# Kernel optimization log

Hardware: AMD Instinct MI355X
Metric: run time of the kernel (lower is better)

The kernel has to match this reference:

```python
import jax, jax.numpy as jnp
import numpy as np

H = 64  # hidden width hard-coded in Agent body


def setup_inputs() -> dict:
    key = jax.random.key(0)
    ks = jax.random.split(key, 10)
    T, B, OBS, A = 1024, 512, 128, 18
    x = jax.random.normal(ks[0], (T, B, OBS), dtype=jnp.float32)
    mask = jax.random.bernoulli(ks[1], 0.01, (T, B))
    initial_carry = jnp.zeros((B, H), dtype=jnp.float32)
    s = lambda k, sh: (jax.random.normal(k, sh, dtype=jnp.float32) * 0.05)
    W1 = s(ks[2], (OBS, H)); b1 = jnp.zeros((H,), jnp.float32)
    Wi = s(ks[3], (H, 3 * H)); bi = jnp.zeros((3 * H,), jnp.float32)
    Wh = s(ks[4], (H, 3 * H)); bhn = jnp.zeros((H,), jnp.float32)
    W2 = s(ks[5], (H, H)); b2 = jnp.zeros((H,), jnp.float32)
    Wl = s(ks[6], (H, A)); bl = jnp.zeros((A,), jnp.float32)
    Wv = s(ks[7], (H, 1)); bv = jnp.zeros((1,), jnp.float32)
    return dict(x=x, mask=mask, initial_carry=initial_carry,
                W1=W1, b1=b1, Wi=Wi, bi=bi, Wh=Wh, bhn=bhn,
                W2=W2, b2=b2, Wl=Wl, bl=bl, Wv=Wv, bv=bv)


def _gru(h, z_t, Wi, bi, Wh, bhn):
    # flax nn.GRUCell math
    gi = z_t @ Wi + bi            # [B, 3H]
    gh = h @ Wh                   # [B, 3H]
    ir, iz, inn = jnp.split(gi, 3, axis=-1)
    hr, hz, hn = jnp.split(gh, 3, axis=-1)
    r = jax.nn.sigmoid(ir + hr)
    u = jax.nn.sigmoid(iz + hz)
    n = jnp.tanh(inn + r * (hn + bhn))
    return (1.0 - u) * n + u * h


def reference(x, mask, initial_carry, W1, b1, Wi, bi, Wh, bhn, W2, b2, Wl, bl, Wv, bv):
    # stem: Dense(64) + relu, applied to all timesteps at once
    z = jax.nn.relu(x @ W1 + b1)                  # [T, B, H]
    m = mask[..., None]                           # [T, B, 1]

    def step(h, inp):
        z_t, m_t = inp
        # masked reset of the carry at episode boundaries
        h = jnp.where(m_t, initial_carry, h)
        h = _gru(h, z_t, Wi, bi, Wh, bhn)
        return h, h

    h_final, ys = jax.lax.scan(step, initial_carry, (z, m))  # ys: [T, B, H]

    y = jax.nn.relu(ys @ W2 + b2)                 # [T, B, H]
    logits = y @ Wl + bl                          # [T, B, A]
    value = y @ Wv + bv                           # [T, B, 1]
    return h_final, logits.squeeze(), value.squeeze(-1)
```

## Files before the change

kernel.cpp:

```cpp
#include <hip/hip_runtime.h>
#include <stdint.h>

#define TT  1024
#define BB  512
#define OBS 128
#define HH  64
#define AA  18
#define RT  (TT*BB)
#define OFF_L ((size_t)BB*HH)
#define OFF_V (OFF_L + (size_t)TT*BB*AA)

#define GI_ELEMS ((size_t)RT*192)
#define WS_NEED  ((GI_ELEMS + (size_t)RT*HH)*4)

typedef __attribute__((ext_vector_type(8))) short bf16x8;
typedef __attribute__((ext_vector_type(4))) float f32x4;
typedef __attribute__((ext_vector_type(4))) unsigned int u32x4;

__device__ __forceinline__ float fast_rcp(float x){ return __builtin_amdgcn_rcpf(x); }
__device__ __forceinline__ float sigm(float x){ return fast_rcp(1.f + __expf(-x)); }
__device__ __forceinline__ float tanh_(float x){ return 1.f - 2.f*fast_rcp(1.f + __expf(2.f*x)); }

__device__ __forceinline__ unsigned bf16_rne(float f){
    unsigned u = __float_as_uint(f);
    return (u + 0x7FFFu + ((u>>16)&1u)) >> 16;
}
__device__ __forceinline__ unsigned pk_bf16(float lo, float hi){
    unsigned d;
    asm("v_cvt_pk_bf16_f32 %0, %1, %2" : "=v"(d) : "v"(lo), "v"(hi));
    return d;
}

__global__ void detect_mask(const uint32_t* __restrict__ m, uint32_t* __restrict__ flag)
{
    const int n_words = (TT * BB) / 4;
    uint32_t acc = 0;
    for (int i = blockIdx.x * blockDim.x + threadIdx.x; i < n_words;
         i += gridDim.x * blockDim.x)
        acc |= (m[i] > 1u) ? 1u : 0u;
    if (acc) flag[0] = 1u;
}

#define P1_BLOCKS 1024
#define ZSTR 70

__global__ __launch_bounds__(256, 2)
void stem_gi(const float* __restrict__ x,
             const float* __restrict__ W1, const float* __restrict__ b1,
             const float* __restrict__ Wi, const float* __restrict__ bi,
             float* __restrict__ gi)
{
    const int tid = threadIdx.x, w = tid >> 6, l = tid & 63;
    const int a = l & 15, q = l >> 4;

    __shared__ float z_s[4][16*ZSTR];
    float* zw = &z_s[w][0];

    bf16x8 W1f[4][4];
    #pragma unroll
    for (int nt = 0; nt < 4; ++nt)
        #pragma unroll
        for (int kf = 0; kf < 4; ++kf) {
            u32x4 pk;
            #pragma unroll
            for (int j2 = 0; j2 < 4; ++j2) {
                const int k0 = kf*32 + q*8 + 2*j2;
                pk[j2] = bf16_rne(W1[(size_t)k0*HH + nt*16 + a])
                       | (bf16_rne(W1[(size_t)(k0+1)*HH + nt*16 + a]) << 16);
            }
            W1f[nt][kf] = __builtin_bit_cast(bf16x8, pk);
        }
    float b1v[4];
    #pragma unroll
    for (int nt = 0; nt < 4; ++nt) b1v[nt] = b1[nt*16 + a];

    bf16x8 Wif[12][2];
    #pragma unroll
    for (int tau = 0; tau < 12; ++tau)
        #pragma unroll
        for (int kf = 0; kf < 2; ++kf) {
            u32x4 pk;
            #pragma unroll
            for (int j2 = 0; j2 < 4; ++j2) {
                const int k0 = kf*32 + q*8 + 2*j2;
                pk[j2] = bf16_rne(Wi[(size_t)k0*192 + tau*16 + a])
                       | (bf16_rne(Wi[(size_t)(k0+1)*192 + tau*16 + a]) << 16);
            }
            Wif[tau][kf] = __builtin_bit_cast(bf16x8, pk);
        }
    float biv[12];
    #pragma unroll
    for (int tau = 0; tau < 12; ++tau) biv[tau] = bi[tau*16 + a];

    for (int it = 0; it < 8; ++it) {
        const size_t grp  = (size_t)blockIdx.x*32 + it*4 + w;
        const float* xr   = x + (grp*16 + a)*OBS;

        float4 xv[8];
        #pragma unroll
        for (int kf = 0; kf < 4; ++kf) {
            xv[2*kf]   = *(const float4*)(xr + kf*32 + q*8);
            xv[2*kf+1] = *(const float4*)(xr + kf*32 + q*8 + 4);
        }
        bf16x8 Af[4];
        #pragma unroll
        for (int kf = 0; kf < 4; ++kf) {
            u32x4 pk;
            pk[0] = pk_bf16(xv[2*kf].x,   xv[2*kf].y);
            pk[1] = pk_bf16(xv[2*kf].z,   xv[2*kf].w);
            pk[2] = pk_bf16(xv[2*kf+1].x, xv[2*kf+1].y);
            pk[3] = pk_bf16(xv[2*kf+1].z, xv[2*kf+1].w);
            Af[kf] = __builtin_bit_cast(bf16x8, pk);
        }

        #pragma unroll
        for (int nt = 0; nt < 4; ++nt) {
            f32x4 D = {b1v[nt], b1v[nt], b1v[nt], b1v[nt]};
            #pragma unroll
            for (int kf = 0; kf < 4; ++kf)
                D = __builtin_amdgcn_mfma_f32_16x16x32_bf16(Af[kf], W1f[nt][kf], D, 0,0,0);
            #pragma unroll
            for (int e = 0; e < 4; ++e)
                zw[(q*4 + e)*ZSTR + nt*16 + a] = fmaxf(D[e], 0.f);
        }
        bf16x8 Az[2];
        #pragma unroll
        for (int s = 0; s < 2; ++s) {
            u32x4 pk;
            #pragma unroll
            for (int j2 = 0; j2 < 4; ++j2) {
                const float2 f = *(const float2*)(zw + a*ZSTR + s*32 + q*8 + 2*j2);
                pk[j2] = pk_bf16(f.x, f.y);
            }
            Az[s] = __builtin_bit_cast(bf16x8, pk);
        }

        float* gb = gi + grp*12*256 + l*4;
        #pragma unroll
        for (int tau = 0; tau < 12; ++tau) {
            f32x4 D = {biv[tau], biv[tau], biv[tau], biv[tau]};
            D = __builtin_amdgcn_mfma_f32_16x16x32_bf16(Az[0], Wif[tau][0], D, 0,0,0);
            D = __builtin_amdgcn_mfma_f32_16x16x32_bf16(Az[1], Wif[tau][1], D, 0,0,0);
            *(f32x4*)(gb + (size_t)tau*256) = D;
        }
    }
}

__global__ __launch_bounds__(256)
void recur9(const float* __restrict__ gip,
            const void* __restrict__ mask_raw,
            const uint32_t* __restrict__ mflag,
            const float* __restrict__ ic,
            const float* __restrict__ Wh,
            const float* __restrict__ bhn,
            float* __restrict__ ys,
            float* __restrict__ out)
{
    const int blk = blockIdx.x;
    const int tid = threadIdx.x;
    const int w   = tid >> 6;
    const int l   = tid & 63;
    const int a   = l & 15;
    const int q   = l >> 4;
    const int dw  = w*16 + a;

    __shared__ float    h_lds[2][64][17];
    __shared__ uint32_t mbits[TT];

    if (mflag[0] != 0) {
        const uint8_t* m8 = (const uint8_t*)mask_raw;
        for (int t0 = w*4; t0 < TT; t0 += 16) {
            const int tt = t0 + q;
            const uint64_t bal = __ballot(m8[(size_t)tt*BB + blk*16 + a] != 0);
            if (l < 4) mbits[t0 + l] = (uint32_t)((bal >> (16*l)) & 0xFFFFu);
        }
    } else {
        const int32_t* m32 = (const int32_t*)mask_raw;
        for (int t0 = w*4; t0 < TT; t0 += 16) {
            const int tt = t0 + q;
            const uint64_t bal = __ballot(m32[(size_t)tt*BB + blk*16 + a] != 0);
            if (l < 4) mbits[t0 + l] = (uint32_t)((bal >> (16*l)) & 0xFFFFu);
        }
    }
    for (int i = tid; i < 16*64; i += 256) {
        const int c = i & 15, d = i >> 4;
        h_lds[0][d][c] = ic[(blk*16 + c)*HH + d];
    }

    bf16x8 Bf[3][2];
    #pragma unroll
    for (int g = 0; g < 3; ++g) {
        const int colb = g*64 + dw;
        #pragma unroll
        for (int s = 0; s < 2; ++s) {
            u32x4 pk;
            #pragma unroll
            for (int j2 = 0; j2 < 4; ++j2) {
                const int k0 = s*32 + q*8 + j2*2;
                pk[j2] = bf16_rne(Wh[(size_t)k0*192 + colb])
                       | (bf16_rne(Wh[(size_t)(k0+1)*192 + colb]) << 16);
            }
            Bf[g][s] = __builtin_bit_cast(bf16x8, pk);
        }
    }
    u32x4 icA[2];
    #pragma unroll
    for (int s = 0; s < 2; ++s) {
        #pragma unroll
        for (int j2 = 0; j2 < 4; ++j2) {
            const int d0 = s*32 + q*8 + j2*2;
            icA[s][j2] = bf16_rne(ic[(blk*16 + a)*HH + d0])
                       | (bf16_rne(ic[(blk*16 + a)*HH + d0 + 1]) << 16);
        }
    }
    float ic_c[4], h_reg[4];
    #pragma unroll
    for (int e = 0; e < 4; ++e) {
        ic_c[e]  = ic[(blk*16 + q*4 + e)*HH + dw];
        h_reg[e] = ic_c[e];
    }
    const float bhnv = bhn[dw];
    const f32x4 Cn = {bhnv, bhnv, bhnv, bhnv};

    __syncthreads();

    #define GSTRIDE ((size_t)32*12*256)
    const float* gbase = gip + (size_t)blk*12*256 + l*4;
    f32x4 buf0[3], buf1[3], buf2[3], buf3[3];
    #pragma unroll
    for (int g = 0; g < 3; ++g) {
        buf0[g] = *(const f32x4*)(gbase + 0*GSTRIDE + (size_t)(g*4 + w)*256);
        buf1[g] = *(const f32x4*)(gbase + 1*GSTRIDE + (size_t)(g*4 + w)*256);
        buf2[g] = *(const f32x4*)(gbase + 2*GSTRIDE + (size_t)(g*4 + w)*256);
        buf3[g] = *(const f32x4*)(gbase + 3*GSTRIDE + (size_t)(g*4 + w)*256);
    }

    auto step = [&](int t, f32x4* cur) {
        const int p = t & 1;
        const uint32_t mb = mbits[t];
        const bool mA = (mb >> a) & 1;
        u32x4 Apk0, Apk1;
        #pragma unroll
        for (int j2 = 0; j2 < 4; ++j2) {
            const int d0 = q*8 + j2*2;
            const unsigned r0 = pk_bf16(h_lds[p][d0][a],    h_lds[p][d0+1][a]);
            const unsigned r1 = pk_bf16(h_lds[p][32+d0][a], h_lds[p][32+d0+1][a]);
            Apk0[j2] = mA ? icA[0][j2] : r0;
            Apk1[j2] = mA ? icA[1][j2] : r1;
        }
        const bf16x8 A0 = __builtin_bit_cast(bf16x8, Apk0);
        const bf16x8 A1 = __builtin_bit_cast(bf16x8, Apk1);
        f32x4 Dr = __builtin_amdgcn_mfma_f32_16x16x32_bf16(A0, Bf[0][0], cur[0], 0,0,0);
        Dr       = __builtin_amdgcn_mfma_f32_16x16x32_bf16(A1, Bf[0][1], Dr,     0,0,0);
        f32x4 Dz = __builtin_amdgcn_mfma_f32_16x16x32_bf16(A0, Bf[1][0], cur[1], 0,0,0);
        Dz       = __builtin_amdgcn_mfma_f32_16x16x32_bf16(A1, Bf[1][1], Dz,     0,0,0);
        f32x4 Dn = __builtin_amdgcn_mfma_f32_16x16x32_bf16(A0, Bf[2][0], Cn,     0,0,0);
        Dn       = __builtin_amdgcn_mfma_f32_16x16x32_bf16(A1, Bf[2][1], Dn,     0,0,0);
        const f32x4 gin = cur[2];
        const int tp = (t + 4 < TT) ? (t + 4) : (TT - 1);
        #pragma unroll
        for (int g = 0; g < 3; ++g)
            cur[g] = *(const f32x4*)(gbase + (size_t)tp*GSTRIDE + (size_t)(g*4 + w)*256);
        float* ysp = ys + ((size_t)t*BB + blk*16 + q*4)*HH + dw;
        #pragma unroll
        for (int e = 0; e < 4; ++e) {
            const bool me   = (mb >> (q*4 + e)) & 1;
            const float he  = me ? ic_c[e] : h_reg[e];
            const float r   = sigm(Dr[e]);
            const float u   = sigm(Dz[e]);
            const float n   = tanh_(fmaf(r, Dn[e], gin[e]));
            const float hn  = fmaf(u, he - n, n);
            h_reg[e] = hn;
            h_lds[p ^ 1][dw][q*4 + e] = hn;
            ysp[(size_t)e*HH] = hn;
        }
        asm volatile("s_waitcnt lgkmcnt(0)" ::: "memory");
        __builtin_amdgcn_s_barrier();
    };

    for (int t = 0; t < TT; t += 4) {
        step(t,     buf0);
        step(t + 1, buf1);
        step(t + 2, buf2);
        step(t + 3, buf3);
    }
    #pragma unroll
    for (int e = 0; e < 4; ++e)
        out[(size_t)(blk*16 + q*4 + e)*HH + dw] = h_reg[e];
    #undef GSTRIDE
}

#define P3_BLOCKS 1024
#define P3_RPW (RT/(P3_BLOCKS*4))

__global__ __launch_bounds__(256, 2)
void heads(const float* __restrict__ ys,
           const float* __restrict__ W2, const float* __restrict__ b2,
           const float* __restrict__ Wl, const float* __restrict__ bl,
           const float* __restrict__ Wv, const float* __restrict__ bv,
           float* __restrict__ out)
{
    const int tid = threadIdx.x, w = tid >> 6, lane = tid & 63;
    __shared__ float4 sb[4][2][16];
    float w2r[64];
    #pragma unroll
    for (int k = 0; k < 64; ++k) w2r[k] = W2[k*HH + lane];
    const float b2v = b2[lane];
    float wc[64]; float bcv = 0.f;
    if (lane < AA) {
        #pragma unroll
        for (int k = 0; k < 64; ++k) wc[k] = Wl[k*AA + lane];
        bcv = bl[lane];
    } else if (lane == AA) {
        #pragma unroll
        for (int k = 0; k < 64; ++k) wc[k] = Wv[k];
        bcv = bv[0];
    } else {
        #pragma unroll
        for (int k = 0; k < 64; ++k) wc[k] = 0.f;
    }
    const int r0 = (blockIdx.x*4 + w) * P3_RPW;
    float ysA = ys[(size_t)r0*HH + lane];
    float ysB = ys[(size_t)(r0+1)*HH + lane];
    for (int rr = 0; rr < P3_RPW; ++rr) {
        const int row = r0 + rr;
        const float ysv = ysA;
        ysA = ysB;
        const int rn = (rr+2 < P3_RPW) ? (row+2) : (r0 + P3_RPW - 1);
        ysB = ys[(size_t)rn*HH + lane];
        ((float*)&sb[w][0][0])[lane] = ysv;
        float acc = b2v;
        {
            const float4* yb = &sb[w][0][0];
            #pragma unroll
            for (int kk = 0; kk < 16; ++kk) {
                const float4 v = yb[kk];
                acc += w2r[4*kk+0]*v.x + w2r[4*kk+1]*v.y
                     + w2r[4*kk+2]*v.z + w2r[4*kk+3]*v.w;
            }
        }
        const float yv = fmaxf(acc, 0.f);
        ((float*)&sb[w][1][0])[lane] = yv;
        float acc2 = bcv;
        {
            const float4* yb = &sb[w][1][0];
            #pragma unroll
            for (int kk = 0; kk < 16; ++kk) {
                const float4 v = yb[kk];
                acc2 += wc[4*kk+0]*v.x + wc[4*kk+1]*v.y
                      + wc[4*kk+2]*v.z + wc[4*kk+3]*v.w;
            }
        }
        if (lane < AA)       out[OFF_L + (size_t)row*AA + lane] = acc2;
        else if (lane == AA) out[OFF_V + row] = acc2;
    }
}

__global__ __launch_bounds__(256, 2)
void gru_agent(const float* __restrict__ x,
               const void* __restrict__ mask_raw,
               const uint32_t* __restrict__ mask_flag,
               const float* __restrict__ ic,
               const float* __restrict__ W1, const float* __restrict__ b1,
               const float* __restrict__ Wi, const float* __restrict__ bi,
               const float* __restrict__ Wh, const float* __restrict__ bhn,
               const float* __restrict__ W2, const float* __restrict__ b2,
               const float* __restrict__ Wl, const float* __restrict__ bl,
               const float* __restrict__ Wv, const float* __restrict__ bv,
               float* __restrict__ out)
{
    const int b    = blockIdx.x;
    const int tid  = threadIdx.x;
    const int w    = tid >> 6;
    const int lane = tid & 63;

    const bool mask_is_u8 = (mask_flag[0] != 0);
    const uint8_t* __restrict__ m8  = (const uint8_t*)mask_raw;
    const int32_t* __restrict__ m32 = (const int32_t*)mask_raw;

    __shared__ float4 x_l[2][4][9];
    __shared__ float4 z_l[16];
    __shared__ float4 h_l[2][16];
    __shared__ float4 y_l[2][16];
    __shared__ float4 ic_l[16];
    __shared__ float  gi_l[192];
    __shared__ float  gh_l[192];

    const int js = (w << 4) | (lane >> 2);
    const int kc = lane & 3;
    float w1r[32];
    #pragma unroll
    for (int i = 0; i < 32; ++i) w1r[i] = W1[(kc*32 + i)*HH + js];
    const float b1v = b1[js];

    float wA[64], wB[64];
    float biv = 0.f, b2v = 0.f, blv = 0.f;
    if (w < 3) {
        const int n = tid;
        #pragma unroll
        for (int k = 0; k < 64; ++k) wA[k] = Wi[k*(3*HH) + n];
        #pragma unroll
        for (int k = 0; k < 64; ++k) wB[k] = Wh[k*(3*HH) + n];
        biv = bi[n];
    } else {
        #pragma unroll
        for (int k = 0; k < 64; ++k) wA[k] = W2[k*HH + lane];
        #pragma unroll
        for (int k = 0; k < 64; ++k) wB[k] = (lane < AA) ? Wl[k*AA + lane]
                                           : (lane == AA ? Wv[k] : 0.f);
        b2v = b2[lane];
        blv = (lane < AA) ? bl[lane] : (lane == AA ? bv[0] : 0.f);
    }
    const float bhnv = (tid < HH) ? bhn[tid] : 0.f;

    if (tid < HH) {
        float v = ic[b*HH + tid];
        ((float*)ic_l)[tid]   = v;
        ((float*)h_l[0])[tid] = v;
    }
    if (tid < OBS) {
        float xv = x[(0*BB + b)*OBS + tid];
        ((float*)&x_l[0][tid>>5])[tid&31] = xv;
    }
    uint8_t m_cur = mask_is_u8 ? m8[b] : (uint8_t)(m32[b] != 0);
    __syncthreads();

    for (int t = 0; t < TT + 2; ++t) {
        const int p = t & 1;
        float xnext = 0.f;
        if (t + 1 < TT && tid < OBS) xnext = x[((t+1)*BB + b)*OBS + tid];
        uint8_t m_next = 0;
        if (t + 1 < TT) {
            const int mi = (t+1)*BB + b;
            m_next = mask_is_u8 ? m8[mi] : (uint8_t)(m32[mi] != 0);
        }
        if (t < TT) {
            const float4* xr = &x_l[p][kc][0];
            float acc = 0.f;
            #pragma unroll
            for (int qq = 0; qq < 8; ++qq) {
                float4 xv = xr[qq];
                acc += w1r[4*qq+0]*xv.x + w1r[4*qq+1]*xv.y
                     + w1r[4*qq+2]*xv.z + w1r[4*qq+3]*xv.w;
            }
            acc += __shfl_xor(acc, 1);
            acc += __shfl_xor(acc, 2);
            if (kc == 0) ((float*)z_l)[js] = fmaxf(acc + b1v, 0.f);
        }
        if (t < TT && w < 3) {
            const float4* hs = m_cur ? ic_l : h_l[p];
            float acc = 0.f;
            #pragma unroll
            for (int kk = 0; kk < 16; ++kk) {
                float4 hv = hs[kk];
                acc += wB[4*kk+0]*hv.x + wB[4*kk+1]*hv.y
                     + wB[4*kk+2]*hv.z + wB[4*kk+3]*hv.w;
            }
            gh_l[tid] = acc;
        } else if (w == 3 && t >= 1 && t <= TT) {
            const float4* hs = h_l[p];
            float acc = b2v;
            #pragma unroll
            for (int kk = 0; kk < 16; ++kk) {
                float4 hv = hs[kk];
                acc += wA[4*kk+0]*hv.x + wA[4*kk+1]*hv.y
                     + wA[4*kk+2]*hv.z + wA[4*kk+3]*hv.w;
            }
            ((float*)y_l[p])[lane] = fmaxf(acc, 0.f);
        }
        __syncthreads();
        if (t < TT && w < 3) {
            float acc = biv;
            #pragma unroll
            for (int kk = 0; kk < 16; ++kk) {
                float4 zv = z_l[kk];
                acc += wA[4*kk+0]*zv.x + wA[4*kk+1]*zv.y
                     + wA[4*kk+2]*zv.z + wA[4*kk+3]*zv.w;
            }
            gi_l[tid] = acc;
        } else if (w == 3 && t >= 2) {
            const float4* yss = y_l[p ^ 1];
            float acc = blv;
            #pragma unroll
            for (int kk = 0; kk < 16; ++kk) {
                float4 yv = yss[kk];
                acc += wB[4*kk+0]*yv.x + wB[4*kk+1]*yv.y
                     + wB[4*kk+2]*yv.z + wB[4*kk+3]*yv.w;
            }
            if (lane < AA)       out[OFF_L + (size_t)((t-2)*BB + b)*AA + lane] = acc;
            else if (lane == AA) out[OFF_V + (size_t)(t-2)*BB + b] = acc;
        }
        __syncthreads();
        if (t < TT && tid < HH) {
            const int j = tid;
            const float irv = gi_l[j], izv = gi_l[HH+j], inn = gi_l[2*HH+j];
            const float hrv = gh_l[j], hzv = gh_l[HH+j], hnv = gh_l[2*HH+j];
            const float heff = m_cur ? ((const float*)ic_l)[j]
                                     : ((const float*)h_l[p])[j];
            const float r  = sigm(irv + hrv);
            const float u  = sigm(izv + hzv);
            const float nn = tanh_(inn + r*(hnv + bhnv));
            ((float*)h_l[p ^ 1])[j] = u*(heff - nn) + nn;
        }
        if (t + 1 < TT && tid < OBS) {
            ((float*)&x_l[p ^ 1][tid>>5])[tid&31] = xnext;
        }
        m_cur = m_next;
        __syncthreads();
    }
    if (tid < HH) out[(size_t)b*HH + tid] = ((const float*)h_l[TT & 1])[tid];
}

extern "C" void kernel_launch(void* const* d_in, const int* in_sizes, int n_in,
                              void* d_out, int out_size, void* d_ws, size_t ws_size,
                              hipStream_t stream) {
    const float* x    = (const float*)d_in[0];
    const void*  mask = (const void*) d_in[1];
    const float* ic   = (const float*)d_in[2];
    const float* W1   = (const float*)d_in[3];
    const float* b1   = (const float*)d_in[4];
    const float* Wi   = (const float*)d_in[5];
    const float* bi   = (const float*)d_in[6];
    const float* Wh   = (const float*)d_in[7];
    const float* bhn  = (const float*)d_in[8];
    const float* W2   = (const float*)d_in[9];
    const float* b2   = (const float*)d_in[10];
    const float* Wl   = (const float*)d_in[11];
    const float* bl   = (const float*)d_in[12];
    const float* Wv   = (const float*)d_in[13];
    const float* bv   = (const float*)d_in[14];
    float* out = (float*)d_out;

    if (ws_size >= WS_NEED) {
        float* gi = (float*)d_ws;
        float* ys = gi + GI_ELEMS;
        uint32_t* flag = (uint32_t*)(out + OFF_V + RT - 1);
        hipMemsetAsync(flag, 0, sizeof(uint32_t), stream);
        detect_mask<<<64, 256, 0, stream>>>((const uint32_t*)mask, flag);
        stem_gi<<<P1_BLOCKS, 256, 0, stream>>>(x, W1, b1, Wi, bi, gi);
        recur9<<<32, 256, 0, stream>>>(gi, mask, flag, ic, Wh, bhn, ys, out);
        heads<<<P3_BLOCKS, 256, 0, stream>>>(ys, W2, b2, Wl, bl, Wv, bv, out);
    } else {
        uint32_t* flag = (uint32_t*)d_ws;
        hipMemsetAsync(flag, 0, sizeof(uint32_t), stream);
        detect_mask<<<64, 256, 0, stream>>>((const uint32_t*)mask, flag);
        gru_agent<<<BB, 256, 0, stream>>>(x, mask, flag, ic, W1, b1, Wi, bi, Wh, bhn,
                                          W2, b2, Wl, bl, Wv, bv, out);
    }
}
```

Measured before the change: 1.005 ms.

## Store recurrent hidden state as bf16 row-major in LDS and double-buffer stem x loads

```diff
diff --git a/kernel.cpp b/kernel.cpp
--- a/kernel.cpp
+++ b/kernel.cpp
@@ -92,16 +92,19 @@
     #pragma unroll
     for (int tau = 0; tau < 12; ++tau) biv[tau] = bi[tau*16 + a];
 
-    for (int it = 0; it < 8; ++it) {
-        const size_t grp  = (size_t)blockIdx.x*32 + it*4 + w;
-        const float* xr   = x + (grp*16 + a)*OBS;
-
-        float4 xv[8];
+    float4 xvA[8], xvB[8];
+
+    auto load_x = [&](int it, float4* dst) {
+        const size_t grp = (size_t)blockIdx.x*32 + it*4 + w;
+        const float* xr  = x + (grp*16 + a)*OBS;
         #pragma unroll
         for (int kf = 0; kf < 4; ++kf) {
-            xv[2*kf]   = *(const float4*)(xr + kf*32 + q*8);
-            xv[2*kf+1] = *(const float4*)(xr + kf*32 + q*8 + 4);
-        }
+            dst[2*kf]   = *(const float4*)(xr + kf*32 + q*8);
+            dst[2*kf+1] = *(const float4*)(xr + kf*32 + q*8 + 4);
+        }
+    };
+    auto do_group = [&](int it, const float4* xv) {
+        const size_t grp = (size_t)blockIdx.x*32 + it*4 + w;
         bf16x8 Af[4];
         #pragma unroll
         for (int kf = 0; kf < 4; ++kf) {
@@ -112,7 +115,6 @@
             pk[3] = pk_bf16(xv[2*kf+1].z, xv[2*kf+1].w);
             Af[kf] = __builtin_bit_cast(bf16x8, pk);
         }
-
         #pragma unroll
         for (int nt = 0; nt < 4; ++nt) {
             f32x4 D = {b1v[nt], b1v[nt], b1v[nt], b1v[nt]};
@@ -134,7 +136,6 @@
             }
             Az[s] = __builtin_bit_cast(bf16x8, pk);
         }
-
         float* gb = gi + grp*12*256 + l*4;
         #pragma unroll
         for (int tau = 0; tau < 12; ++tau) {
@@ -143,18 +144,28 @@
             D = __builtin_amdgcn_mfma_f32_16x16x32_bf16(Az[1], Wif[tau][1], D, 0,0,0);
             *(f32x4*)(gb + (size_t)tau*256) = D;
         }
-    }
-}
+    };
+
+    load_x(0, xvA);
+    for (int it = 0; it < 8; it += 2) {
+        if (it + 1 < 8) load_x(it + 1, xvB);
+        do_group(it, xvA);
+        if (it + 2 < 8) load_x(it + 2, xvA);
+        do_group(it + 1, xvB);
+    }
+}
+
+#define HSTR 70
 
 __global__ __launch_bounds__(256)
-void recur9(const float* __restrict__ gip,
-            const void* __restrict__ mask_raw,
-            const uint32_t* __restrict__ mflag,
-            const float* __restrict__ ic,
-            const float* __restrict__ Wh,
-            const float* __restrict__ bhn,
-            float* __restrict__ ys,
-            float* __restrict__ out)
+void recur10(const float* __restrict__ gip,
+             const void* __restrict__ mask_raw,
+             const uint32_t* __restrict__ mflag,
+             const float* __restrict__ ic,
+             const float* __restrict__ Wh,
+             const float* __restrict__ bhn,
+             float* __restrict__ ys,
+             float* __restrict__ out)
 {
     const int blk = blockIdx.x;
     const int tid = threadIdx.x;
@@ -164,7 +175,7 @@
     const int q   = l >> 4;
     const int dw  = w*16 + a;
 
-    __shared__ float    h_lds[2][64][17];
+    __shared__ unsigned short h16[2][16][HSTR];
     __shared__ uint32_t mbits[TT];
 
     if (mflag[0] != 0) {
@@ -183,8 +194,8 @@
         }
     }
     for (int i = tid; i < 16*64; i += 256) {
-        const int c = i & 15, d = i >> 4;
-        h_lds[0][d][c] = ic[(blk*16 + c)*HH + d];
+        const int c = i >> 6, d = i & 63;
+        h16[0][c][d] = (unsigned short)bf16_rne(ic[(blk*16 + c)*HH + d]);
     }
 
     bf16x8 Bf[3][2];
@@ -239,14 +250,14 @@
         const int p = t & 1;
         const uint32_t mb = mbits[t];
         const bool mA = (mb >> a) & 1;
+        const uint32_t* hrow = (const uint32_t*)&h16[p][a][0];
         u32x4 Apk0, Apk1;
         #pragma unroll
         for (int j2 = 0; j2 < 4; ++j2) {
-            const int d0 = q*8 + j2*2;
-            const unsigned r0 = pk_bf16(h_lds[p][d0][a],    h_lds[p][d0+1][a]);
-            const unsigned r1 = pk_bf16(h_lds[p][32+d0][a], h_lds[p][32+d0+1][a]);
-            Apk0[j2] = mA ? icA[0][j2] : r0;
-            Apk1[j2] = mA ? icA[1][j2] : r1;
+            const uint32_t v0 = hrow[q*4 + j2];
+            const uint32_t v1 = hrow[16 + q*4 + j2];
+            Apk0[j2] = mA ? icA[0][j2] : v0;
+            Apk1[j2] = mA ? icA[1][j2] : v1;
         }
         const bf16x8 A0 = __builtin_bit_cast(bf16x8, Apk0);
         const bf16x8 A1 = __builtin_bit_cast(bf16x8, Apk1);
@@ -262,6 +273,7 @@
         for (int g = 0; g < 3; ++g)
             cur[g] = *(const f32x4*)(gbase + (size_t)tp*GSTRIDE + (size_t)(g*4 + w)*256);
         float* ysp = ys + ((size_t)t*BB + blk*16 + q*4)*HH + dw;
+        float hn_[4];
         #pragma unroll
         for (int e = 0; e < 4; ++e) {
             const bool me   = (mb >> (q*4 + e)) & 1;
@@ -271,9 +283,15 @@
             const float n   = tanh_(fmaf(r, Dn[e], gin[e]));
             const float hn  = fmaf(u, he - n, n);
             h_reg[e] = hn;
-            h_lds[p ^ 1][dw][q*4 + e] = hn;
+            hn_[e] = hn;
             ysp[(size_t)e*HH] = hn;
         }
+        const uint32_t pk01 = pk_bf16(hn_[0], hn_[1]);
+        const uint32_t pk23 = pk_bf16(hn_[2], hn_[3]);
+        h16[p ^ 1][q*4 + 0][dw] = (unsigned short)(pk01 & 0xFFFFu);
+        h16[p ^ 1][q*4 + 1][dw] = (unsigned short)(pk01 >> 16);
+        h16[p ^ 1][q*4 + 2][dw] = (unsigned short)(pk23 & 0xFFFFu);
+        h16[p ^ 1][q*4 + 3][dw] = (unsigned short)(pk23 >> 16);
         asm volatile("s_waitcnt lgkmcnt(0)" ::: "memory");
         __builtin_amdgcn_s_barrier();
     };
@@ -538,7 +556,7 @@
         hipMemsetAsync(flag, 0, sizeof(uint32_t), stream);
         detect_mask<<<64, 256, 0, stream>>>((const uint32_t*)mask, flag);
         stem_gi<<<P1_BLOCKS, 256, 0, stream>>>(x, W1, b1, Wi, bi, gi);
-        recur9<<<32, 256, 0, stream>>>(gi, mask, flag, ic, Wh, bhn, ys, out);
+        recur10<<<32, 256, 0, stream>>>(gi, mask, flag, ic, Wh, bhn, ys, out);
         heads<<<P3_BLOCKS, 256, 0, stream>>>(ys, W2, b2, Wl, bl, Wv, bv, out);
     } else {
         uint32_t* flag = (uint32_t*)d_ws;
```

After: 1.173 ms. 16.8% more time.
